# Kernel tuning notes

Measured on AMD Instinct MI355X. Metric: run time of the kernel, lower is better.

## Reference

```python
import jax, jax.numpy as jnp
import numpy as np

SMOOTH = 1e-07
LAMBDA = 0.1


def setup_inputs() -> dict:
    key = jax.random.key(0)
    k1, k2, k3 = jax.random.split(key, 3)
    B, C, S, H, W = 8, 12, 4, 512, 512
    superclass_scores = jax.random.uniform(k1, (B, S, H, W), dtype=jnp.float32)
    class_score = jax.random.uniform(k2, (B, C, H, W), dtype=jnp.float32)
    weights = jnp.ones((C,), dtype=jnp.float32)
    target = jax.random.randint(k3, (B, H, W), 0, C, dtype=jnp.int32)
    # super2sub = [[0,1,2],[3,4,5],[6,7,8],[9,10,11]] -> class j belongs to superclass j//3
    sub2super = (jnp.arange(C, dtype=jnp.int32) // 3).astype(jnp.int32)
    return {
        "superclass_scores": superclass_scores,
        "class_score": class_score,
        "weights": weights,
        "target": target,
        "sub2super": sub2super,
    }


def _dice_sum(scores, one_hot):
    # scores, one_hot: [B, K, H, W]; per-class dice over all pixels & batch
    inter = jnp.sum(scores * one_hot, axis=(0, 2, 3))            # [K]
    isum = jnp.sum(scores, axis=(0, 2, 3))                       # [K]
    tsum = jnp.sum(one_hot, axis=(0, 2, 3))                      # [K]
    return 1.0 - (2.0 * inter + SMOOTH) / (isum + tsum + SMOOTH)  # [K]


def reference(superclass_scores, class_score, weights, target, sub2super):
    B, C, H, W = class_score.shape
    S = superclass_scores.shape[1]

    # super_target[b,h,w] = superclass of target[b,h,w]
    super_target = sub2super[target]                              # [B,H,W]

    # one-hot encodings (channel-major, like scatter_ on dim=1)
    cls_ids = jnp.arange(C, dtype=target.dtype)
    target_one_hot = (target[:, None] == cls_ids[None, :, None, None]).astype(class_score.dtype)  # [B,C,H,W]
    sup_ids = jnp.arange(S, dtype=target.dtype)
    super_one_hot = (super_target[:, None] == sup_ids[None, :, None, None]).astype(class_score.dtype)  # [B,S,H,W]

    super_class_loss = jnp.sum(_dice_sum(superclass_scores, super_one_hot))
    final_class_loss = jnp.sum(_dice_sum(class_score, target_one_hot) * weights)

    loss = LAMBDA * super_class_loss / S + final_class_loss / jnp.sum(weights)

    # final_class_score[:, j] = class_score[:, j] * superclass_scores[:, sub2super[j]]
    final_class_score = class_score * superclass_scores[:, sub2super, :, :]

    return (loss, final_class_score, target_one_hot)
```

## Files before the change

### kernel.cpp

```cpp
#include <hip/hip_runtime.h>

#define SMOOTH_F 1e-7f

typedef float f32x4 __attribute__((ext_vector_type(4)));

constexpr int B = 8, C = 12, S = 4, H = 512, W = 512;
constexpr int HW    = H * W;
constexpr int NPIX  = B * HW;
constexpr int QUADS = NPIX / 4;
constexpr int BLOCK = 256;
constexpr int GRID  = 1024;
constexpr int ITERS = QUADS / (GRID * BLOCK);

constexpr int NSUMS = 48;

__global__ __launch_bounds__(BLOCK, 4) void fused_kernel(
    const float* __restrict__ ss,
    const float* __restrict__ cs,
    const int*   __restrict__ tgt,
    const int*   __restrict__ s2s,
    float* __restrict__ out_fc,
    float* __restrict__ out_oh,
    float* __restrict__ sums)
{
    const int tid = blockIdx.x * BLOCK + threadIdx.x;

    float interS[S] = {0.f, 0.f, 0.f, 0.f};
    float isumS[S]  = {0.f, 0.f, 0.f, 0.f};
    float interC[C] = {0.f};
    float isumC[C]  = {0.f};
    int   tS[S]     = {0};
    int   tC[C]     = {0};

    #pragma unroll
    for (int it = 0; it < ITERS; ++it) {
        const int q   = tid + it * (GRID * BLOCK);
        const int p   = q << 2;
        const int b   = p >> 18;
        const int rem = p & (HW - 1);

        const int4 t4 = *reinterpret_cast<const int4*>(tgt + p);
        const int t[4] = {t4.x, t4.y, t4.z, t4.w};
        int st[4];
        #pragma unroll
        for (int i = 0; i < 4; i++) st[i] = s2s[t[i]];

        float ssv[S][4];
        #pragma unroll
        for (int s = 0; s < S; s++) {
            const float4 v = *reinterpret_cast<const float4*>(ss + (b * S + s) * HW + rem);
            ssv[s][0] = v.x; ssv[s][1] = v.y; ssv[s][2] = v.z; ssv[s][3] = v.w;
            isumS[s] += v.x + v.y + v.z + v.w;
            #pragma unroll
            for (int i = 0; i < 4; i++) {
                const bool m = (st[i] == s);
                interS[s] += m ? ssv[s][i] : 0.f;
                tS[s] += (int)__popcll(__ballot(m));
            }
        }

        float cv[C][4];
        #pragma unroll
        for (int c = 0; c < C; c++) {
            const float4 v = *reinterpret_cast<const float4*>(cs + (b * C + c) * HW + rem);
            cv[c][0] = v.x; cv[c][1] = v.y; cv[c][2] = v.z; cv[c][3] = v.w;
        }

        #pragma unroll
        for (int c = 0; c < C; c++) {
            const int base = (b * C + c) * HW + rem;
            const int sup  = s2s[c];
            isumC[c] += cv[c][0] + cv[c][1] + cv[c][2] + cv[c][3];
            f32x4 oh4, fc4;
            #pragma unroll
            for (int i = 0; i < 4; i++) {
                const bool eq = (t[i] == c);
                const float ohv = eq ? 1.f : 0.f;
                const float sv = (sup == 0) ? ssv[0][i]
                               : (sup == 1) ? ssv[1][i]
                               : (sup == 2) ? ssv[2][i]
                               :              ssv[3][i];
                oh4[i] = ohv;
                fc4[i] = cv[c][i] * sv;
                interC[c] += eq ? cv[c][i] : 0.f;
                tC[c] += (int)__popcll(__ballot(eq));
            }
            __builtin_nontemporal_store(oh4, reinterpret_cast<f32x4*>(out_oh + base));
            __builtin_nontemporal_store(fc4, reinterpret_cast<f32x4*>(out_fc + base));
        }
    }

    float vals[32];
    #pragma unroll
    for (int s = 0; s < S; s++) { vals[s] = interS[s]; vals[4 + s] = isumS[s]; }
    #pragma unroll
    for (int c = 0; c < C; c++) { vals[8 + c] = interC[c]; vals[20 + c] = isumC[c]; }

    __shared__ float red[BLOCK / 64][NSUMS];
    const int lane = threadIdx.x & 63;
    const int wv   = threadIdx.x >> 6;

    #pragma unroll
    for (int k = 0; k < 32; k++) {
        float v = vals[k];
        #pragma unroll
        for (int o = 32; o > 0; o >>= 1) v += __shfl_xor(v, o, 64);
        if (lane == 0) {
            const int idx = (k < 8) ? k : (k < 20) ? (12 + (k - 8)) : (24 + (k - 20));
            red[wv][idx] = v;
        }
    }
    if (lane == 0) {
        #pragma unroll
        for (int s = 0; s < S; s++) red[wv][8 + s]  = (float)tS[s];
        #pragma unroll
        for (int c = 0; c < C; c++) red[wv][36 + c] = (float)tC[c];
    }
    __syncthreads();
    if (threadIdx.x < NSUMS) {
        const float sblk = red[0][threadIdx.x] + red[1][threadIdx.x]
                         + red[2][threadIdx.x] + red[3][threadIdx.x];
        atomicAdd(&sums[threadIdx.x], sblk);
    }
}

__global__ void loss_kernel(const float* __restrict__ sums,
                            const float* __restrict__ w,
                            float* __restrict__ out)
{
    if (threadIdx.x == 0 && blockIdx.x == 0) {
        float superL = 0.f;
        #pragma unroll
        for (int s = 0; s < S; s++)
            superL += 1.f - (2.f * sums[s] + SMOOTH_F) / (sums[4 + s] + sums[8 + s] + SMOOTH_F);
        float finalL = 0.f, wsum = 0.f;
        #pragma unroll
        for (int c = 0; c < C; c++) {
            wsum   += w[c];
            finalL += w[c] * (1.f - (2.f * sums[12 + c] + SMOOTH_F) / (sums[24 + c] + sums[36 + c] + SMOOTH_F));
        }
        out[0] = 0.1f * superL / (float)S + finalL / wsum;
    }
}

extern "C" void kernel_launch(void* const* d_in, const int* in_sizes, int n_in,
                              void* d_out, int out_size, void* d_ws, size_t ws_size,
                              hipStream_t stream) {
    const float* ss  = (const float*)d_in[0];
    const float* cs  = (const float*)d_in[1];
    const float* w   = (const float*)d_in[2];
    const int*   tgt = (const int*)d_in[3];
    const int*   s2s = (const int*)d_in[4];

    float* out    = (float*)d_out;
    float* out_fc = out + 1;
    float* out_oh = out + 1 + (size_t)B * C * HW;
    float* sums   = (float*)d_ws;

    hipMemsetAsync(sums, 0, NSUMS * sizeof(float), stream);
    fused_kernel<<<GRID, BLOCK, 0, stream>>>(ss, cs, tgt, s2s, out_fc, out_oh, sums);
    loss_kernel<<<1, 64, 0, stream>>>(sums, w, out);
}
```

Baseline: 99.78 us.

## Launch one thread per pixel quad and drop the grid-stride loop

Removes the per-thread iteration loop so each thread handles exactly one quad of pixels, and raises the grid from 1024 blocks to QUADS/BLOCK (2048). The launch-bounds occupancy hint goes from 4 to 8, and the output stores switch from nontemporal to regular stores. Each block still does a full shared-memory reduction plus 48 atomics, so the number of atomic operations doubles. Lower register pressure may allow more waves to be resident to hide latency.

```diff
diff --git a/kernel.cpp b/kernel.cpp
--- a/kernel.cpp
+++ b/kernel.cpp
@@ -9,12 +9,11 @@
 constexpr int NPIX  = B * HW;
 constexpr int QUADS = NPIX / 4;
 constexpr int BLOCK = 256;
-constexpr int GRID  = 1024;
-constexpr int ITERS = QUADS / (GRID * BLOCK);
+constexpr int GRID  = QUADS / BLOCK;
 
 constexpr int NSUMS = 48;
 
-__global__ __launch_bounds__(BLOCK, 4) void fused_kernel(
+__global__ __launch_bounds__(BLOCK, 8) void fused_kernel(
     const float* __restrict__ ss,
     const float* __restrict__ cs,
     const int*   __restrict__ tgt,
@@ -23,71 +22,65 @@
     float* __restrict__ out_oh,
     float* __restrict__ sums)
 {
-    const int tid = blockIdx.x * BLOCK + threadIdx.x;
+    const int q   = blockIdx.x * BLOCK + threadIdx.x;
+    const int p   = q << 2;
+    const int b   = p >> 18;
+    const int rem = p & (HW - 1);
 
-    float interS[S] = {0.f, 0.f, 0.f, 0.f};
-    float isumS[S]  = {0.f, 0.f, 0.f, 0.f};
-    float interC[C] = {0.f};
-    float isumC[C]  = {0.f};
-    int   tS[S]     = {0};
-    int   tC[C]     = {0};
+    float interS[S], isumS[S];
+    float interC[C], isumC[C];
+    int   tS[S];
+    int   tC[C];
+
+    const int4 t4 = *reinterpret_cast<const int4*>(tgt + p);
+    const int t[4] = {t4.x, t4.y, t4.z, t4.w};
+    int st[4];
+    #pragma unroll
+    for (int i = 0; i < 4; i++) st[i] = s2s[t[i]];
+
+    float ssv[S][4];
+    #pragma unroll
+    for (int s = 0; s < S; s++) {
+        const float4 v = *reinterpret_cast<const float4*>(ss + (b * S + s) * HW + rem);
+        ssv[s][0] = v.x; ssv[s][1] = v.y; ssv[s][2] = v.z; ssv[s][3] = v.w;
+        isumS[s] = v.x + v.y + v.z + v.w;
+        interS[s] = 0.f; tS[s] = 0;
+        #pragma unroll
+        for (int i = 0; i < 4; i++) {
+            const bool m = (st[i] == s);
+            interS[s] += m ? ssv[s][i] : 0.f;
+            tS[s] += (int)__popcll(__ballot(m));
+        }
+    }
+
+    float cv[C][4];
+    #pragma unroll
+    for (int c = 0; c < C; c++) {
+        const float4 v = *reinterpret_cast<const float4*>(cs + (b * C + c) * HW + rem);
+        cv[c][0] = v.x; cv[c][1] = v.y; cv[c][2] = v.z; cv[c][3] = v.w;
+    }
 
     #pragma unroll
-    for (int it = 0; it < ITERS; ++it) {
-        const int q   = tid + it * (GRID * BLOCK);
-        const int p   = q << 2;
-        const int b   = p >> 18;
-        const int rem = p & (HW - 1);
-
-        const int4 t4 = *reinterpret_cast<const int4*>(tgt + p);
-        const int t[4] = {t4.x, t4.y, t4.z, t4.w};
-        int st[4];
+    for (int c = 0; c < C; c++) {
+        const int base = (b * C + c) * HW + rem;
+        const int sup  = s2s[c];
+        isumC[c] = cv[c][0] + cv[c][1] + cv[c][2] + cv[c][3];
+        interC[c] = 0.f; tC[c] = 0;
+        f32x4 oh4, fc4;
         #pragma unroll
-        for (int i = 0; i < 4; i++) st[i] = s2s[t[i]];
-
-        float ssv[S][4];
-        #pragma unroll
-        for (int s = 0; s < S; s++) {
-            const float4 v = *reinterpret_cast<const float4*>(ss + (b * S + s) * HW + rem);
-            ssv[s][0] = v.x; ssv[s][1] = v.y; ssv[s][2] = v.z; ssv[s][3] = v.w;
-            isumS[s] += v.x + v.y + v.z + v.w;
-            #pragma unroll
-            for (int i = 0; i < 4; i++) {
-                const bool m = (st[i] == s);
-                interS[s] += m ? ssv[s][i] : 0.f;
-                tS[s] += (int)__popcll(__ballot(m));
-            }
+        for (int i = 0; i < 4; i++) {
+            const bool eq = (t[i] == c);
+            const float sv = (sup == 0) ? ssv[0][i]
+                           : (sup == 1) ? ssv[1][i]
+                           : (sup == 2) ? ssv[2][i]
+                           :              ssv[3][i];
+            oh4[i] = eq ? 1.f : 0.f;
+            fc4[i] = cv[c][i] * sv;
+            interC[c] += eq ? cv[c][i] : 0.f;
+            tC[c] += (int)__popcll(__ballot(eq));
         }
-
-        float cv[C][4];
-        #pragma unroll
-        for (int c = 0; c < C; c++) {
-            const float4 v = *reinterpret_cast<const float4*>(cs + (b * C + c) * HW + rem);
-            cv[c][0] = v.x; cv[c][1] = v.y; cv[c][2] = v.z; cv[c][3] = v.w;
-        }
-
-        #pragma unroll
-        for (int c = 0; c < C; c++) {
-            const int base = (b * C + c) * HW + rem;
-            const int sup  = s2s[c];
-            isumC[c] += cv[c][0] + cv[c][1] + cv[c][2] + cv[c][3];
-            f32x4 oh4, fc4;
-            #pragma unroll
-            for (int i = 0; i < 4; i++) {
-                const bool eq = (t[i] == c);
-                const float ohv = eq ? 1.f : 0.f;
-                const float sv = (sup == 0) ? ssv[0][i]
-                               : (sup == 1) ? ssv[1][i]
-                               : (sup == 2) ? ssv[2][i]
-                               :              ssv[3][i];
-                oh4[i] = ohv;
-                fc4[i] = cv[c][i] * sv;
-                interC[c] += eq ? cv[c][i] : 0.f;
-                tC[c] += (int)__popcll(__ballot(eq));
-            }
-            __builtin_nontemporal_store(oh4, reinterpret_cast<f32x4*>(out_oh + base));
-            __builtin_nontemporal_store(fc4, reinterpret_cast<f32x4*>(out_fc + base));
-        }
+        *reinterpret_cast<f32x4*>(out_oh + base) = oh4;
+        *reinterpret_cast<f32x4*>(out_fc + base) = fc4;
     }
 
     float vals[32];
```

Result: slower. 135.4 us (+35.7%).
